# Kernel optimization log

Hardware: AMD Instinct MI355X
Metric: run time of the kernel (lower is better)

## Reference

```python
import jax, jax.numpy as jnp
import numpy as np

N = 2048          # num nodes
C = 256           # dense_dim per input
EMB = 3 * C       # 768
H = 8             # num_heads
D = EMB // H      # 96 head_dim
ALPHA = 0.2       # leaky relu slope
SCALE = D ** -0.5


def setup_inputs() -> dict:
    key = jax.random.key(0)
    ks = jax.random.split(key, 9)
    sd = EMB ** -0.5
    return {
        "eh": jax.random.normal(ks[0], (N, C), jnp.float32),
        "er": jax.random.normal(ks[1], (N, C), jnp.float32),
        "et": jax.random.normal(ks[2], (N, C), jnp.float32),
        "h_id": jax.random.randint(ks[3], (N,), 0, 32),
        "W_w": jax.random.normal(ks[4], (EMB, EMB), jnp.float32) * sd,
        "a": jax.random.normal(ks[5], (2 * D, 1), jnp.float32) * (2 * D) ** -0.5,
        "proj_w": jax.random.normal(ks[6], (EMB, EMB), jnp.float32) * sd,
        "proj_b": jnp.zeros((EMB,), jnp.float32),
        "skip_w": jax.random.normal(ks[7], (EMB, EMB), jnp.float32) * sd,
        "skip_b": jnp.zeros((EMB,), jnp.float32),
    }


def reference(eh, er, et, h_id, W_w, a, proj_w, proj_b, skip_w, skip_b):
    n = eh.shape[0]
    e = jnp.concatenate([eh, er, et], axis=-1)            # [N, EMB]
    Wh = (e @ W_w.T).reshape(n, H, D)                     # [N, H, D]

    # score = leakyrelu(a1 . Wh_scrambled[i] + a2 . Wh[j]) * scale
    a1, a2 = a[:D, 0], a[D:, 0]
    s1 = Wh @ a1                                          # [N, H]
    s2 = Wh @ a2                                          # [N, H]
    # torch's Wh.repeat(1,1,N).view(N*N,H,D) reads head (j*H + h)//N for pair (i,j,h)
    qidx = (jnp.arange(n)[:, None] * H + jnp.arange(H)[None, :]) // n  # [N, H]
    x = s1[:, qidx] + s2[None, :, :]                      # [N, N, H]
    e_ij = jnp.where(x >= 0, x, ALPHA * x) * SCALE

    mask = h_id[:, None] != h_id[None, :]                 # [N, N]
    e_ij = jnp.where(mask[:, :, None], -jnp.inf, e_ij)
    attn = jax.nn.softmax(e_ij, axis=1)                   # softmax over neighbors j

    out = jnp.einsum('ijh,jhd->ihd', attn, Wh).reshape(n, H * D)
    out = out @ proj_w.T + proj_b                         # [N, EMB]
    skip = e @ skip_w.T + skip_b                          # [N, EMB]
    return skip + out
```

## Files before the change

kernel.cpp:

```cpp
#include <hip/hip_runtime.h>
#include <hip/hip_bf16.h>

#define N_NODES 2048
#define EMB 768
#define NH 8
#define DH 96
#define ALPHA 0.2f
#define SCALE 0.10206207261596575f
#define NGMAX 192
#define WSZ (EMB * EMB)

typedef __bf16 bf16x8 __attribute__((ext_vector_type(8)));
typedef float f32x4 __attribute__((ext_vector_type(4)));
typedef __attribute__((address_space(3))) unsigned int lds_u32;
typedef __attribute__((address_space(1))) const unsigned int glb_u32;

union pack4 { ushort4 u; __hip_bfloat16 h[4]; };

__global__ __launch_bounds__(256) void prep_kernel(
    const float* __restrict__ eh, const float* __restrict__ er, const float* __restrict__ et,
    const float* __restrict__ W0, const float* __restrict__ W1, const float* __restrict__ W2,
    __hip_bfloat16* __restrict__ e, __hip_bfloat16* __restrict__ o0,
    __hip_bfloat16* __restrict__ o1, __hip_bfloat16* __restrict__ o2, int* __restrict__ cnt)
{
    const int b = blockIdx.x;
    const int gtid = b * 256 + threadIdx.x;
    if (gtid < 32) cnt[gtid] = 0;
    const float* src;
    __hip_bfloat16* dst;
    if (b < 1536) {
        int idx = gtid * 4;
        int i = idx / EMB, c = idx % EMB;
        if (c < 256)      src = eh + i * 256 + c;
        else if (c < 512) src = er + i * 256 + (c - 256);
        else              src = et + i * 256 + (c - 512);
        dst = e + (size_t)i * EMB + c;
    } else {
        int idx = (gtid - 1536 * 256) * 4;
        if (idx < WSZ)          { src = W0 + idx;           dst = o0 + idx; }
        else if (idx < 2 * WSZ) { src = W1 + idx - WSZ;     dst = o1 + idx - WSZ; }
        else                    { src = W2 + idx - 2 * WSZ; dst = o2 + idx - 2 * WSZ; }
    }
    float4 v = *reinterpret_cast<const float4*>(src);
    pack4 p;
    p.h[0] = __float2bfloat16(v.x);
    p.h[1] = __float2bfloat16(v.y);
    p.h[2] = __float2bfloat16(v.z);
    p.h[3] = __float2bfloat16(v.w);
    *reinterpret_cast<ushort4*>(dst) = p.u;
}

__device__ __forceinline__ void stageA64(
    const __hip_bfloat16* __restrict__ src, int row0, int k0,
    __hip_bfloat16* lds, int wave, int lane)
{
#pragma unroll
    for (int i = 0; i < 4; i++) {
        const int c0 = wave * 256 + i * 64;
        const int c = c0 + lane;
        const int row = c >> 3;
        const int cb = (c & 7) ^ (row & 7);
        const __hip_bfloat16* g = src + (size_t)(row0 + row) * EMB + k0 + cb * 8;
        __builtin_amdgcn_global_load_lds((glb_u32*)g, (lds_u32*)(lds + c0 * 8), 16, 0, 0);
    }
}
__device__ __forceinline__ void stageB64(
    const __hip_bfloat16* __restrict__ src, int row0, int k0,
    __hip_bfloat16* lds, int wave, int lane)
{
#pragma unroll
    for (int i = 0; i < 2; i++) {
        const int c0 = wave * 128 + i * 64;
        const int c = c0 + lane;
        const int row = c >> 3;
        const int cb = (c & 7) ^ (row & 7);
        const __hip_bfloat16* g = src + (size_t)(row0 + row) * EMB + k0 + cb * 8;
        __builtin_amdgcn_global_load_lds((glb_u32*)g, (lds_u32*)(lds + c0 * 8), 16, 0, 0);
    }
}

__global__ __launch_bounds__(256) void gemm_kernel(
    const __hip_bfloat16* __restrict__ A,
    const __hip_bfloat16* __restrict__ B1, const __hip_bfloat16* __restrict__ B2,
    const float* __restrict__ bias1, const float* __restrict__ bias2,
    float* __restrict__ C1, float* __restrict__ C2,
    int nbn1, int accum)
{
    __shared__ __attribute__((aligned(16))) __hip_bfloat16 smA[3][8192];
    __shared__ __attribute__((aligned(16))) __hip_bfloat16 smB[3][4096];

    const int t = threadIdx.x;
    const int lane = t & 63, wave = t >> 6;
    const int wm = wave >> 1, wn = wave & 1;
    const int bnb = blockIdx.x;
    const bool second = bnb >= nbn1;
    const __hip_bfloat16* B = second ? B2 : B1;
    float* Cf = second ? C2 : C1;
    const int bn = (second ? bnb - nbn1 : bnb) * 64;
    const int bm = blockIdx.y * 128;
    const int l15 = lane & 15, quad = lane >> 4;

    f32x4 acc00 = {0,0,0,0}, acc01 = {0,0,0,0};
    f32x4 acc10 = {0,0,0,0}, acc11 = {0,0,0,0};
    f32x4 acc20 = {0,0,0,0}, acc21 = {0,0,0,0};
    f32x4 acc30 = {0,0,0,0}, acc31 = {0,0,0,0};

    const int ra0 = wm * 64 + l15;
    const int rb0 = wn * 32 + l15;
    const int xa = ra0 & 7;
    const int xb = rb0 & 7;

    stageA64(A, bm, 0, &smA[0][0], wave, lane);
    stageB64(B, bn, 0, &smB[0][0], wave, lane);

    int bufc = 0;
#pragma unroll 1
    for (int s = 0; s < 12; s++) {
        const int bufn = (bufc == 2) ? 0 : bufc + 1;
        if (s + 1 < 12) {
            const int k0 = (s + 1) * 64;
            stageA64(A, bm, k0, &smA[bufn][0], wave, lane);
            stageB64(B, bn, k0, &smB[bufn][0], wave, lane);
            asm volatile("s_waitcnt vmcnt(6)" ::: "memory");
        } else {
            asm volatile("s_waitcnt vmcnt(0)" ::: "memory");
        }
        __builtin_amdgcn_s_barrier();

        const __hip_bfloat16* At = &smA[bufc][0];
        const __hip_bfloat16* Bt = &smB[bufc][0];
#pragma unroll
        for (int ks = 0; ks < 2; ks++) {
            const int cq = ks * 4 + quad;
            bf16x8 a0 = *(const bf16x8*)(At + (size_t)((ra0     ) * 8 + (cq ^ xa)) * 8);
            bf16x8 a1 = *(const bf16x8*)(At + (size_t)((ra0 + 16) * 8 + (cq ^ xa)) * 8);
            bf16x8 a2 = *(const bf16x8*)(At + (size_t)((ra0 + 32) * 8 + (cq ^ xa)) * 8);
            bf16x8 a3 = *(const bf16x8*)(At + (size_t)((ra0 + 48) * 8 + (cq ^ xa)) * 8);
            bf16x8 b0 = *(const bf16x8*)(Bt + (size_t)((rb0     ) * 8 + (cq ^ xb)) * 8);
            bf16x8 b1 = *(const bf16x8*)(Bt + (size_t)((rb0 + 16) * 8 + (cq ^ xb)) * 8);
            acc00 = __builtin_amdgcn_mfma_f32_16x16x32_bf16(a0, b0, acc00, 0, 0, 0);
            acc01 = __builtin_amdgcn_mfma_f32_16x16x32_bf16(a0, b1, acc01, 0, 0, 0);
            acc10 = __builtin_amdgcn_mfma_f32_16x16x32_bf16(a1, b0, acc10, 0, 0, 0);
            acc11 = __builtin_amdgcn_mfma_f32_16x16x32_bf16(a1, b1, acc11, 0, 0, 0);
            acc20 = __builtin_amdgcn_mfma_f32_16x16x32_bf16(a2, b0, acc20, 0, 0, 0);
            acc21 = __builtin_amdgcn_mfma_f32_16x16x32_bf16(a2, b1, acc21, 0, 0, 0);
            acc30 = __builtin_amdgcn_mfma_f32_16x16x32_bf16(a3, b0, acc30, 0, 0, 0);
            acc31 = __builtin_amdgcn_mfma_f32_16x16x32_bf16(a3, b1, acc31, 0, 0, 0);
        }
        bufc = bufn;
    }

    const int col0 = bn + wn * 32 + l15;
    const int col1 = col0 + 16;
    float bv0 = 0.f, bv1 = 0.f;
    if (second && bias1 != nullptr) {
        bv0 = bias1[col0] + bias2[col0];
        bv1 = bias1[col1] + bias2[col1];
    }
    const int r0 = bm + wm * 64 + quad * 4;
#pragma unroll
    for (int r = 0; r < 4; r++) {
        const int rw0 = r0 + r, rw1 = rw0 + 16, rw2 = rw0 + 32, rw3 = rw0 + 48;
        float* p00 = &Cf[(size_t)rw0 * EMB + col0]; float* p01 = &Cf[(size_t)rw0 * EMB + col1];
        float* p10 = &Cf[(size_t)rw1 * EMB + col0]; float* p11 = &Cf[(size_t)rw1 * EMB + col1];
        float* p20 = &Cf[(size_t)rw2 * EMB + col0]; float* p21 = &Cf[(size_t)rw2 * EMB + col1];
        float* p30 = &Cf[(size_t)rw3 * EMB + col0]; float* p31 = &Cf[(size_t)rw3 * EMB + col1];
        if (accum) {
            *p00 += acc00[r]; *p01 += acc01[r];
            *p10 += acc10[r]; *p11 += acc11[r];
            *p20 += acc20[r]; *p21 += acc21[r];
            *p30 += acc30[r]; *p31 += acc31[r];
        } else {
            *p00 = acc00[r] + bv0; *p01 = acc01[r] + bv1;
            *p10 = acc10[r] + bv0; *p11 = acc11[r] + bv1;
            *p20 = acc20[r] + bv0; *p21 = acc21[r] + bv1;
            *p30 = acc30[r] + bv0; *p31 = acc31[r] + bv1;
        }
    }
}

__global__ __launch_bounds__(256) void s12g_kernel(
    const float* __restrict__ Wh, const float* __restrict__ a,
    float* __restrict__ s1, float* __restrict__ s2,
    const int* __restrict__ h_id, int* __restrict__ cnt, int* __restrict__ lists)
{
    int gid = blockIdx.x * 256 + threadIdx.x;
    if (gid < N_NODES) {
        int g = h_id[gid];
        int p = atomicAdd(&cnt[g], 1);
        lists[g * N_NODES + p] = gid;
    }
    int i = gid >> 3, h = gid & 7;
    const float* wr = Wh + (size_t)i * EMB + h * DH;
    float acc1 = 0.f, acc2 = 0.f;
    for (int d = 0; d < DH; d++) {
        float w = wr[d];
        acc1 += w * a[d];
        acc2 += w * a[DH + d];
    }
    s1[gid] = acc1;
    s2[gid] = acc2;
}

__global__ __launch_bounds__(256) void attn_kernel(
    const float* __restrict__ Wh, const float* __restrict__ s1, const float* __restrict__ s2,
    const int* __restrict__ cnt, const int* __restrict__ lists,
    __hip_bfloat16* __restrict__ out)
{
    const int g  = blockIdx.x & 31;
    const int h  = (blockIdx.x >> 5) & 7;
    const int dh = blockIdx.x >> 8;
    const int t  = threadIdx.x;

    __shared__ int   jb[NGMAX];
    __shared__ int   qg[NGMAX];
    __shared__ float s2g[NGMAX];
    __shared__ float s1g[NGMAX][9];
    __shared__ float Whg[NGMAX][48];

    const int ng = min(cnt[g], NGMAX);
    const int* gl = lists + g * N_NODES;

    for (int j = t; j < ng; j += 256) {
        int node = gl[j];
        jb[j]  = node;
        qg[j]  = node >> 8;
        s2g[j] = s2[node * 8 + h];
        float4 v0 = *reinterpret_cast<const float4*>(s1 + node * 8);
        float4 v1 = *reinterpret_cast<const float4*>(s1 + node * 8 + 4);
        s1g[j][0] = v0.x; s1g[j][1] = v0.y; s1g[j][2] = v0.z; s1g[j][3] = v0.w;
        s1g[j][4] = v1.x; s1g[j][5] = v1.y; s1g[j][6] = v1.z; s1g[j][7] = v1.w;
    }
    __syncthreads();
    for (int idx = t; idx < ng * 12; idx += 256) {
        int jc = idx / 12, dq = idx % 12;
        float4 v = *reinterpret_cast<const float4*>(
            Wh + (size_t)jb[jc] * EMB + h * DH + dh * 48 + dq * 4);
        *reinterpret_cast<float4*>(&Whg[jc][dq * 4]) = v;
    }
    __syncthreads();

    const int half = t >> 7;
    const int d0 = half * 24;
    for (int tr = t & 127; tr < ng; tr += 128) {
        float m = -1e30f;
        for (int j = 0; j < ng; j++) {
            float x = s1g[tr][qg[j]] + s2g[j];
            float ev = (x >= 0.f ? x : ALPHA * x) * SCALE;
            m = fmaxf(m, ev);
        }
        float S = 0.f;
        for (int j = 0; j < ng; j++) {
            float x = s1g[tr][qg[j]] + s2g[j];
            float ev = (x >= 0.f ? x : ALPHA * x) * SCALE;
            S += __expf(ev - m);
        }
        const float ri = 1.f / S;

        float acc[24];
#pragma unroll
        for (int d = 0; d < 24; d++) acc[d] = 0.f;
        for (int j = 0; j < ng; j++) {
            float x = s1g[tr][qg[j]] + s2g[j];
            float ev = (x >= 0.f ? x : ALPHA * x) * SCALE;
            float p = __expf(ev - m) * ri;
#pragma unroll
            for (int d = 0; d < 24; d++) acc[d] += p * Whg[j][d0 + d];
        }
        __hip_bfloat16* po = out + (size_t)jb[tr] * EMB + h * DH + dh * 48 + d0;
#pragma unroll
        for (int d = 0; d < 24; d += 4) {
            pack4 pk;
            pk.h[0] = __float2bfloat16(acc[d]);
            pk.h[1] = __float2bfloat16(acc[d + 1]);
            pk.h[2] = __float2bfloat16(acc[d + 2]);
            pk.h[3] = __float2bfloat16(acc[d + 3]);
            *reinterpret_cast<ushort4*>(po + d) = pk.u;
        }
    }
}

extern "C" void kernel_launch(void* const* d_in, const int* in_sizes, int n_in,
                              void* d_out, int out_size, void* d_ws, size_t ws_size,
                              hipStream_t stream)
{
    const float* eh     = (const float*)d_in[0];
    const float* er     = (const float*)d_in[1];
    const float* et     = (const float*)d_in[2];
    const int*   h_id   = (const int*)d_in[3];
    const float* W_w    = (const float*)d_in[4];
    const float* a      = (const float*)d_in[5];
    const float* proj_w = (const float*)d_in[6];
    const float* proj_b = (const float*)d_in[7];
    const float* skip_w = (const float*)d_in[8];
    const float* skip_b = (const float*)d_in[9];
    float* out = (float*)d_out;

    char* ws = (char*)d_ws;
    __hip_bfloat16* e_ws   = (__hip_bfloat16*)(ws);
    float*          Wh_ws  = (float*)(ws + 3145728);
    __hip_bfloat16* at_ws  = (__hip_bfloat16*)(ws + 9437184);
    __hip_bfloat16* Wb_ws  = (__hip_bfloat16*)(ws + 12582912);
    __hip_bfloat16* Pb_ws  = (__hip_bfloat16*)(ws + 13762560);
    __hip_bfloat16* Sb_ws  = (__hip_bfloat16*)(ws + 14942208);
    float*          s1_ws  = (float*)(ws + 16121856);
    float*          s2_ws  = (float*)(ws + 16187392);
    int*            cnt_ws = (int*)(ws + 16252928);
    int*            lst_ws = (int*)(ws + 16253056);

    prep_kernel<<<3264, 256, 0, stream>>>(eh, er, et, W_w, proj_w, skip_w,
                                          e_ws, Wb_ws, Pb_ws, Sb_ws, cnt_ws);

    gemm_kernel<<<dim3(24, 16), 256, 0, stream>>>(
        e_ws, Wb_ws, Sb_ws, proj_b, skip_b, Wh_ws, out, 12, 0);

    s12g_kernel<<<64, 256, 0, stream>>>(Wh_ws, a, s1_ws, s2_ws, h_id, cnt_ws, lst_ws);

    attn_kernel<<<512, 256, 0, stream>>>(Wh_ws, s1_ws, s2_ws, cnt_ws, lst_ws, at_ws);

    gemm_kernel<<<dim3(12, 16), 256, 0, stream>>>(
        at_ws, Pb_ws, nullptr, nullptr, nullptr, out, nullptr, 12, 1);
}
```

Before: 137.3 us.

## Fuse all stages into one persistent kernel with grid barriers

Replaces the five separate launches with a single 512-block persistent kernel that runs prep/convert, both GEMMs, attention and the projection GEMM as phases separated by atomic grid barriers. The s1/s2 attention scores are now computed in the first GEMM's epilogue via shuffle reductions and atomics, and the per-group node lists are built deterministically by one block instead of atomic appends. This removes launch gaps and a separate scoring pass. In exchange it relies on all 512 blocks being co-resident (2 per CU with 72KB of LDS each), and it idles many blocks during the GEMM phases.

```diff
diff --git a/kernel.cpp b/kernel.cpp
--- a/kernel.cpp
+++ b/kernel.cpp
@@ -9,6 +9,7 @@
 #define SCALE 0.10206207261596575f
 #define NGMAX 192
 #define WSZ (EMB * EMB)
+#define NBLK 512u
 
 typedef __bf16 bf16x8 __attribute__((ext_vector_type(8)));
 typedef float f32x4 __attribute__((ext_vector_type(4)));
@@ -17,37 +18,20 @@
 
 union pack4 { ushort4 u; __hip_bfloat16 h[4]; };
 
-__global__ __launch_bounds__(256) void prep_kernel(
-    const float* __restrict__ eh, const float* __restrict__ er, const float* __restrict__ et,
-    const float* __restrict__ W0, const float* __restrict__ W1, const float* __restrict__ W2,
-    __hip_bfloat16* __restrict__ e, __hip_bfloat16* __restrict__ o0,
-    __hip_bfloat16* __restrict__ o1, __hip_bfloat16* __restrict__ o2, int* __restrict__ cnt)
-{
-    const int b = blockIdx.x;
-    const int gtid = b * 256 + threadIdx.x;
-    if (gtid < 32) cnt[gtid] = 0;
-    const float* src;
-    __hip_bfloat16* dst;
-    if (b < 1536) {
-        int idx = gtid * 4;
-        int i = idx / EMB, c = idx % EMB;
-        if (c < 256)      src = eh + i * 256 + c;
-        else if (c < 512) src = er + i * 256 + (c - 256);
-        else              src = et + i * 256 + (c - 512);
-        dst = e + (size_t)i * EMB + c;
-    } else {
-        int idx = (gtid - 1536 * 256) * 4;
-        if (idx < WSZ)          { src = W0 + idx;           dst = o0 + idx; }
-        else if (idx < 2 * WSZ) { src = W1 + idx - WSZ;     dst = o1 + idx - WSZ; }
-        else                    { src = W2 + idx - 2 * WSZ; dst = o2 + idx - 2 * WSZ; }
-    }
-    float4 v = *reinterpret_cast<const float4*>(src);
-    pack4 p;
-    p.h[0] = __float2bfloat16(v.x);
-    p.h[1] = __float2bfloat16(v.y);
-    p.h[2] = __float2bfloat16(v.z);
-    p.h[3] = __float2bfloat16(v.w);
-    *reinterpret_cast<ushort4*>(dst) = p.u;
+__device__ __forceinline__ void grid_barrier(unsigned* bar, unsigned target)
+{
+    __syncthreads();
+    if (threadIdx.x == 0) {
+        __threadfence();
+        atomicAdd(bar, 1u);
+        int guard = 0;
+        while (atomicAdd(bar, 0u) < target && guard < (1 << 22)) {
+            __builtin_amdgcn_s_sleep(1);
+            guard++;
+        }
+        __threadfence();
+    }
+    __syncthreads();
 }
 
 __device__ __forceinline__ void stageA64(
@@ -79,39 +63,28 @@
     }
 }
 
-__global__ __launch_bounds__(256) void gemm_kernel(
-    const __hip_bfloat16* __restrict__ A,
-    const __hip_bfloat16* __restrict__ B1, const __hip_bfloat16* __restrict__ B2,
+__device__ __forceinline__ void gemm_phase(
+    const __hip_bfloat16* __restrict__ A, const __hip_bfloat16* __restrict__ B,
+    float* __restrict__ Cf, int bm, int bn,
     const float* __restrict__ bias1, const float* __restrict__ bias2,
-    float* __restrict__ C1, float* __restrict__ C2,
-    int nbn1, int accum)
-{
-    __shared__ __attribute__((aligned(16))) __hip_bfloat16 smA[3][8192];
-    __shared__ __attribute__((aligned(16))) __hip_bfloat16 smB[3][4096];
-
-    const int t = threadIdx.x;
-    const int lane = t & 63, wave = t >> 6;
+    int accum,
+    const float* __restrict__ avec, float* __restrict__ s1, float* __restrict__ s2,
+    __hip_bfloat16* smA, __hip_bfloat16* smB, int lane, int wave)
+{
     const int wm = wave >> 1, wn = wave & 1;
-    const int bnb = blockIdx.x;
-    const bool second = bnb >= nbn1;
-    const __hip_bfloat16* B = second ? B2 : B1;
-    float* Cf = second ? C2 : C1;
-    const int bn = (second ? bnb - nbn1 : bnb) * 64;
-    const int bm = blockIdx.y * 128;
     const int l15 = lane & 15, quad = lane >> 4;
 
-    f32x4 acc00 = {0,0,0,0}, acc01 = {0,0,0,0};
-    f32x4 acc10 = {0,0,0,0}, acc11 = {0,0,0,0};
-    f32x4 acc20 = {0,0,0,0}, acc21 = {0,0,0,0};
-    f32x4 acc30 = {0,0,0,0}, acc31 = {0,0,0,0};
+    f32x4 acc[4][2];
+#pragma unroll
+    for (int k = 0; k < 4; k++) { acc[k][0] = f32x4{0,0,0,0}; acc[k][1] = f32x4{0,0,0,0}; }
 
     const int ra0 = wm * 64 + l15;
     const int rb0 = wn * 32 + l15;
     const int xa = ra0 & 7;
     const int xb = rb0 & 7;
 
-    stageA64(A, bm, 0, &smA[0][0], wave, lane);
-    stageB64(B, bn, 0, &smB[0][0], wave, lane);
+    stageA64(A, bm, 0, smA, wave, lane);
+    stageB64(B, bn, 0, smB, wave, lane);
 
     int bufc = 0;
 #pragma unroll 1
@@ -119,33 +92,27 @@
         const int bufn = (bufc == 2) ? 0 : bufc + 1;
         if (s + 1 < 12) {
             const int k0 = (s + 1) * 64;
-            stageA64(A, bm, k0, &smA[bufn][0], wave, lane);
-            stageB64(B, bn, k0, &smB[bufn][0], wave, lane);
+            stageA64(A, bm, k0, smA + bufn * 8192, wave, lane);
+            stageB64(B, bn, k0, smB + bufn * 4096, wave, lane);
             asm volatile("s_waitcnt vmcnt(6)" ::: "memory");
         } else {
             asm volatile("s_waitcnt vmcnt(0)" ::: "memory");
         }
         __builtin_amdgcn_s_barrier();
 
-        const __hip_bfloat16* At = &smA[bufc][0];
-        const __hip_bfloat16* Bt = &smB[bufc][0];
+        const __hip_bfloat16* At = smA + bufc * 8192;
+        const __hip_bfloat16* Bt = smB + bufc * 4096;
 #pragma unroll
         for (int ks = 0; ks < 2; ks++) {
             const int cq = ks * 4 + quad;
-            bf16x8 a0 = *(const bf16x8*)(At + (size_t)((ra0     ) * 8 + (cq ^ xa)) * 8);
-            bf16x8 a1 = *(const bf16x8*)(At + (size_t)((ra0 + 16) * 8 + (cq ^ xa)) * 8);
-            bf16x8 a2 = *(const bf16x8*)(At + (size_t)((ra0 + 32) * 8 + (cq ^ xa)) * 8);
-            bf16x8 a3 = *(const bf16x8*)(At + (size_t)((ra0 + 48) * 8 + (cq ^ xa)) * 8);
             bf16x8 b0 = *(const bf16x8*)(Bt + (size_t)((rb0     ) * 8 + (cq ^ xb)) * 8);
             bf16x8 b1 = *(const bf16x8*)(Bt + (size_t)((rb0 + 16) * 8 + (cq ^ xb)) * 8);
-            acc00 = __builtin_amdgcn_mfma_f32_16x16x32_bf16(a0, b0, acc00, 0, 0, 0);
-            acc01 = __builtin_amdgcn_mfma_f32_16x16x32_bf16(a0, b1, acc01, 0, 0, 0);
-            acc10 = __builtin_amdgcn_mfma_f32_16x16x32_bf16(a1, b0, acc10, 0, 0, 0);
-            acc11 = __builtin_amdgcn_mfma_f32_16x16x32_bf16(a1, b1, acc11, 0, 0, 0);
-            acc20 = __builtin_amdgcn_mfma_f32_16x16x32_bf16(a2, b0, acc20, 0, 0, 0);
-            acc21 = __builtin_amdgcn_mfma_f32_16x16x32_bf16(a2, b1, acc21, 0, 0, 0);
-            acc30 = __builtin_amdgcn_mfma_f32_16x16x32_bf16(a3, b0, acc30, 0, 0, 0);
-            acc31 = __builtin_amdgcn_mfma_f32_16x16x32_bf16(a3, b1, acc31, 0, 0, 0);
+#pragma unroll
+            for (int k = 0; k < 4; k++) {
+                bf16x8 av = *(const bf16x8*)(At + (size_t)((ra0 + 16 * k) * 8 + (cq ^ xa)) * 8);
+                acc[k][0] = __builtin_amdgcn_mfma_f32_16x16x32_bf16(av, b0, acc[k][0], 0, 0, 0);
+                acc[k][1] = __builtin_amdgcn_mfma_f32_16x16x32_bf16(av, b1, acc[k][1], 0, 0, 0);
+            }
         }
         bufc = bufn;
     }
@@ -153,130 +120,213 @@
     const int col0 = bn + wn * 32 + l15;
     const int col1 = col0 + 16;
     float bv0 = 0.f, bv1 = 0.f;
-    if (second && bias1 != nullptr) {
+    if (bias1 != nullptr) {
         bv0 = bias1[col0] + bias2[col0];
         bv1 = bias1[col1] + bias2[col1];
     }
     const int r0 = bm + wm * 64 + quad * 4;
 #pragma unroll
-    for (int r = 0; r < 4; r++) {
-        const int rw0 = r0 + r, rw1 = rw0 + 16, rw2 = rw0 + 32, rw3 = rw0 + 48;
-        float* p00 = &Cf[(size_t)rw0 * EMB + col0]; float* p01 = &Cf[(size_t)rw0 * EMB + col1];
-        float* p10 = &Cf[(size_t)rw1 * EMB + col0]; float* p11 = &Cf[(size_t)rw1 * EMB + col1];
-        float* p20 = &Cf[(size_t)rw2 * EMB + col0]; float* p21 = &Cf[(size_t)rw2 * EMB + col1];
-        float* p30 = &Cf[(size_t)rw3 * EMB + col0]; float* p31 = &Cf[(size_t)rw3 * EMB + col1];
-        if (accum) {
-            *p00 += acc00[r]; *p01 += acc01[r];
-            *p10 += acc10[r]; *p11 += acc11[r];
-            *p20 += acc20[r]; *p21 += acc21[r];
-            *p30 += acc30[r]; *p31 += acc31[r];
+    for (int k = 0; k < 4; k++) {
+#pragma unroll
+        for (int r = 0; r < 4; r++) {
+            const int row = r0 + 16 * k + r;
+            float* p0 = &Cf[(size_t)row * EMB + col0];
+            float* p1 = &Cf[(size_t)row * EMB + col1];
+            if (accum) { *p0 += acc[k][0][r]; *p1 += acc[k][1][r]; }
+            else       { *p0 = acc[k][0][r] + bv0; *p1 = acc[k][1][r] + bv1; }
+        }
+    }
+
+    if (avec != nullptr) {
+        const int cb0 = bn + wn * 32;
+        const int h = cb0 / DH;
+        const int ch = cb0 % DH + l15;
+        const float a10 = avec[ch],      a11 = avec[ch + 16];
+        const float a20 = avec[DH + ch], a21 = avec[DH + ch + 16];
+#pragma unroll
+        for (int k = 0; k < 4; k++) {
+#pragma unroll
+            for (int r = 0; r < 4; r++) {
+                float v1 = acc[k][0][r] * a10 + acc[k][1][r] * a11;
+                float v2 = acc[k][0][r] * a20 + acc[k][1][r] * a21;
+#pragma unroll
+                for (int m = 1; m < 16; m <<= 1) {
+                    v1 += __shfl_xor(v1, m);
+                    v2 += __shfl_xor(v2, m);
+                }
+                if (l15 == 0) {
+                    const int row = r0 + 16 * k + r;
+                    atomicAdd(&s1[row * NH + h], v1);
+                    atomicAdd(&s2[row * NH + h], v2);
+                }
+            }
+        }
+    }
+}
+
+__global__ __launch_bounds__(256, 2) void mega_kernel(
+    const float* __restrict__ eh, const float* __restrict__ er, const float* __restrict__ et,
+    const int* __restrict__ h_id, const float* __restrict__ a,
+    const float* __restrict__ proj_b, const float* __restrict__ skip_b,
+    const float* __restrict__ W_w, const float* __restrict__ proj_w, const float* __restrict__ skip_w,
+    __hip_bfloat16* __restrict__ e, __hip_bfloat16* __restrict__ Wb,
+    __hip_bfloat16* __restrict__ Pb, __hip_bfloat16* __restrict__ Sb,
+    float* __restrict__ Wh, float* __restrict__ s1, float* __restrict__ s2,
+    int* __restrict__ cnt, int* __restrict__ lists,
+    __hip_bfloat16* __restrict__ at, float* __restrict__ out,
+    unsigned* __restrict__ bar)
+{
+    __shared__ __attribute__((aligned(16))) char lds_raw[73728];
+
+    const int bid = blockIdx.x;
+    const int t = threadIdx.x;
+    const int lane = t & 63, wave = t >> 6;
+
+    {
+        const float4 z4 = {0.f, 0.f, 0.f, 0.f};
+        for (int i = bid * 256 + t; i < 843776; i += 512 * 256) {
+            if (i < 393216) {
+                const int idx = i * 4;
+                const int row = idx / EMB, c = idx % EMB;
+                const float* src;
+                if (c < 256)      src = eh + row * 256 + c;
+                else if (c < 512) src = er + row * 256 + (c - 256);
+                else              src = et + row * 256 + (c - 512);
+                float4 v = *reinterpret_cast<const float4*>(src);
+                pack4 p;
+                p.h[0] = __float2bfloat16(v.x); p.h[1] = __float2bfloat16(v.y);
+                p.h[2] = __float2bfloat16(v.z); p.h[3] = __float2bfloat16(v.w);
+                *reinterpret_cast<ushort4*>(e + (size_t)row * EMB + c) = p.u;
+            } else if (i < 835584) {
+                const int w = i - 393216;
+                const int which = w / 147456;
+                const int off = (w % 147456) * 4;
+                const float* src = (which == 0 ? W_w : which == 1 ? proj_w : skip_w) + off;
+                __hip_bfloat16* dst = (which == 0 ? Wb : which == 1 ? Pb : Sb) + off;
+                float4 v = *reinterpret_cast<const float4*>(src);
+                pack4 p;
+                p.h[0] = __float2bfloat16(v.x); p.h[1] = __float2bfloat16(v.y);
+                p.h[2] = __float2bfloat16(v.z); p.h[3] = __float2bfloat16(v.w);
+                *reinterpret_cast<ushort4*>(dst) = p.u;
+            } else {
+                reinterpret_cast<float4*>(s1)[i - 835584] = z4;
+            }
+        }
+        if (bid == 511) {
+            int* hh = (int*)lds_raw;
+            int (*seg)[8] = (int(*)[8])(lds_raw + 8192);
+            for (int j = t; j < N_NODES; j += 256) hh[j] = h_id[j];
+            __syncthreads();
+            const int g = t >> 3, sgt = t & 7;
+            int c = 0;
+            for (int j = sgt * 256; j < sgt * 256 + 256; j++) c += (hh[j] == g) ? 1 : 0;
+            seg[g][sgt] = c;
+            __syncthreads();
+            int off = 0;
+            for (int k = 0; k < sgt; k++) off += seg[g][k];
+            int p = off;
+            for (int j = sgt * 256; j < sgt * 256 + 256; j++)
+                if (hh[j] == g) lists[g * N_NODES + (p++)] = j;
+            if (sgt == 7) cnt[g] = off + c;
+        }
+    }
+    grid_barrier(bar, NBLK);
+
+    if (bid < 384) {
+        const int bnb = bid % 24, bmb = bid / 24;
+        const int bm = bmb * 128;
+        __hip_bfloat16* smA = (__hip_bfloat16*)lds_raw;
+        __hip_bfloat16* smB = (__hip_bfloat16*)(lds_raw + 49152);
+        if (bnb < 12) {
+            gemm_phase(e, Wb, Wh, bm, bnb * 64, nullptr, nullptr, 0,
+                       a, s1, s2, smA, smB, lane, wave);
         } else {
-            *p00 = acc00[r] + bv0; *p01 = acc01[r] + bv1;
-            *p10 = acc10[r] + bv0; *p11 = acc11[r] + bv1;
-            *p20 = acc20[r] + bv0; *p21 = acc21[r] + bv1;
-            *p30 = acc30[r] + bv0; *p31 = acc31[r] + bv1;
-        }
-    }
-}
-
-__global__ __launch_bounds__(256) void s12g_kernel(
-    const float* __restrict__ Wh, const float* __restrict__ a,
-    float* __restrict__ s1, float* __restrict__ s2,
-    const int* __restrict__ h_id, int* __restrict__ cnt, int* __restrict__ lists)
-{
-    int gid = blockIdx.x * 256 + threadIdx.x;
-    if (gid < N_NODES) {
-        int g = h_id[gid];
-        int p = atomicAdd(&cnt[g], 1);
-        lists[g * N_NODES + p] = gid;
-    }
-    int i = gid >> 3, h = gid & 7;
-    const float* wr = Wh + (size_t)i * EMB + h * DH;
-    float acc1 = 0.f, acc2 = 0.f;
-    for (int d = 0; d < DH; d++) {
-        float w = wr[d];
-        acc1 += w * a[d];
-        acc2 += w * a[DH + d];
-    }
-    s1[gid] = acc1;
-    s2[gid] = acc2;
-}
-
-__global__ __launch_bounds__(256) void attn_kernel(
-    const float* __restrict__ Wh, const float* __restrict__ s1, const float* __restrict__ s2,
-    const int* __restrict__ cnt, const int* __restrict__ lists,
-    __hip_bfloat16* __restrict__ out)
-{
-    const int g  = blockIdx.x & 31;
-    const int h  = (blockIdx.x >> 5) & 7;
-    const int dh = blockIdx.x >> 8;
-    const int t  = threadIdx.x;
-
-    __shared__ int   jb[NGMAX];
-    __shared__ int   qg[NGMAX];
-    __shared__ float s2g[NGMAX];
-    __shared__ float s1g[NGMAX][9];
-    __shared__ float Whg[NGMAX][48];
-
-    const int ng = min(cnt[g], NGMAX);
-    const int* gl = lists + g * N_NODES;
-
-    for (int j = t; j < ng; j += 256) {
-        int node = gl[j];
-        jb[j]  = node;
-        qg[j]  = node >> 8;
-        s2g[j] = s2[node * 8 + h];
-        float4 v0 = *reinterpret_cast<const float4*>(s1 + node * 8);
-        float4 v1 = *reinterpret_cast<const float4*>(s1 + node * 8 + 4);
-        s1g[j][0] = v0.x; s1g[j][1] = v0.y; s1g[j][2] = v0.z; s1g[j][3] = v0.w;
-        s1g[j][4] = v1.x; s1g[j][5] = v1.y; s1g[j][6] = v1.z; s1g[j][7] = v1.w;
-    }
-    __syncthreads();
-    for (int idx = t; idx < ng * 12; idx += 256) {
-        int jc = idx / 12, dq = idx % 12;
-        float4 v = *reinterpret_cast<const float4*>(
-            Wh + (size_t)jb[jc] * EMB + h * DH + dh * 48 + dq * 4);
-        *reinterpret_cast<float4*>(&Whg[jc][dq * 4]) = v;
-    }
-    __syncthreads();
-
-    const int half = t >> 7;
-    const int d0 = half * 24;
-    for (int tr = t & 127; tr < ng; tr += 128) {
-        float m = -1e30f;
-        for (int j = 0; j < ng; j++) {
-            float x = s1g[tr][qg[j]] + s2g[j];
-            float ev = (x >= 0.f ? x : ALPHA * x) * SCALE;
-            m = fmaxf(m, ev);
-        }
-        float S = 0.f;
-        for (int j = 0; j < ng; j++) {
-            float x = s1g[tr][qg[j]] + s2g[j];
-            float ev = (x >= 0.f ? x : ALPHA * x) * SCALE;
-            S += __expf(ev - m);
-        }
-        const float ri = 1.f / S;
-
-        float acc[24];
-#pragma unroll
-        for (int d = 0; d < 24; d++) acc[d] = 0.f;
-        for (int j = 0; j < ng; j++) {
-            float x = s1g[tr][qg[j]] + s2g[j];
-            float ev = (x >= 0.f ? x : ALPHA * x) * SCALE;
-            float p = __expf(ev - m) * ri;
-#pragma unroll
-            for (int d = 0; d < 24; d++) acc[d] += p * Whg[j][d0 + d];
-        }
-        __hip_bfloat16* po = out + (size_t)jb[tr] * EMB + h * DH + dh * 48 + d0;
-#pragma unroll
-        for (int d = 0; d < 24; d += 4) {
-            pack4 pk;
-            pk.h[0] = __float2bfloat16(acc[d]);
-            pk.h[1] = __float2bfloat16(acc[d + 1]);
-            pk.h[2] = __float2bfloat16(acc[d + 2]);
-            pk.h[3] = __float2bfloat16(acc[d + 3]);
-            *reinterpret_cast<ushort4*>(po + d) = pk.u;
-        }
+            gemm_phase(e, Sb, out, bm, (bnb - 12) * 64, proj_b, skip_b, 0,
+                       nullptr, nullptr, nullptr, smA, smB, lane, wave);
+        }
+    }
+    grid_barrier(bar, 2 * NBLK);
+
+    {
+        const int g  = bid & 31;
+        const int h  = (bid >> 5) & 7;
+        const int dh = bid >> 8;
+
+        int*   jb  = (int*)lds_raw;
+        int*   qg  = (int*)(lds_raw + 768);
+        float* s2g = (float*)(lds_raw + 1536);
+        float (*s1g)[9]  = (float(*)[9])(lds_raw + 2304);
+        float (*Whg)[48] = (float(*)[48])(lds_raw + 9216);
+
+        const int ng = min(cnt[g], NGMAX);
+        const int* gl = lists + g * N_NODES;
+
+        for (int j = t; j < ng; j += 256) {
+            int node = gl[j];
+            jb[j]  = node;
+            qg[j]  = node >> 8;
+            s2g[j] = s2[node * 8 + h];
+            float4 v0 = *reinterpret_cast<const float4*>(s1 + node * 8);
+            float4 v1 = *reinterpret_cast<const float4*>(s1 + node * 8 + 4);
+            s1g[j][0] = v0.x; s1g[j][1] = v0.y; s1g[j][2] = v0.z; s1g[j][3] = v0.w;
+            s1g[j][4] = v1.x; s1g[j][5] = v1.y; s1g[j][6] = v1.z; s1g[j][7] = v1.w;
+        }
+        __syncthreads();
+        for (int idx = t; idx < ng * 12; idx += 256) {
+            int jc = idx / 12, dq = idx % 12;
+            float4 v = *reinterpret_cast<const float4*>(
+                Wh + (size_t)jb[jc] * EMB + h * DH + dh * 48 + dq * 4);
+            *reinterpret_cast<float4*>(&Whg[jc][dq * 4]) = v;
+        }
+        __syncthreads();
+
+        const int half = t >> 7;
+        const int d0 = half * 24;
+        for (int tr = t & 127; tr < ng; tr += 128) {
+            float m = -1e30f;
+            for (int j = 0; j < ng; j++) {
+                float x = s1g[tr][qg[j]] + s2g[j];
+                float ev = (x >= 0.f ? x : ALPHA * x) * SCALE;
+                m = fmaxf(m, ev);
+            }
+            float S = 0.f;
+            for (int j = 0; j < ng; j++) {
+                float x = s1g[tr][qg[j]] + s2g[j];
+                float ev = (x >= 0.f ? x : ALPHA * x) * SCALE;
+                S += __expf(ev - m);
+            }
+            const float ri = 1.f / S;
+
+            float acc[24];
+#pragma unroll
+            for (int d = 0; d < 24; d++) acc[d] = 0.f;
+            for (int j = 0; j < ng; j++) {
+                float x = s1g[tr][qg[j]] + s2g[j];
+                float ev = (x >= 0.f ? x : ALPHA * x) * SCALE;
+                float p = __expf(ev - m) * ri;
+#pragma unroll
+                for (int d = 0; d < 24; d++) acc[d] += p * Whg[j][d0 + d];
+            }
+            __hip_bfloat16* po = at + (size_t)jb[tr] * EMB + h * DH + dh * 48 + d0;
+#pragma unroll
+            for (int d = 0; d < 24; d += 4) {
+                pack4 pk;
+                pk.h[0] = __float2bfloat16(acc[d]);
+                pk.h[1] = __float2bfloat16(acc[d + 1]);
+                pk.h[2] = __float2bfloat16(acc[d + 2]);
+                pk.h[3] = __float2bfloat16(acc[d + 3]);
+                *reinterpret_cast<ushort4*>(po + d) = pk.u;
+            }
+        }
+    }
+    grid_barrier(bar, 3 * NBLK);
+
+    if (bid < 192) {
+        const int bnb = bid % 12, bmb = bid / 12;
+        __hip_bfloat16* smA = (__hip_bfloat16*)lds_raw;
+        __hip_bfloat16* smB = (__hip_bfloat16*)(lds_raw + 49152);
+        gemm_phase(at, Pb, out, bmb * 128, bnb * 64, nullptr, nullptr, 1,
+                   nullptr, nullptr, nullptr, smA, smB, lane, wave);
     }
 }
 
@@ -307,17 +357,12 @@
     float*          s2_ws  = (float*)(ws + 16187392);
     int*            cnt_ws = (int*)(ws + 16252928);
     int*            lst_ws = (int*)(ws + 16253056);
-
-    prep_kernel<<<3264, 256, 0, stream>>>(eh, er, et, W_w, proj_w, skip_w,
-                                          e_ws, Wb_ws, Pb_ws, Sb_ws, cnt_ws);
-
-    gemm_kernel<<<dim3(24, 16), 256, 0, stream>>>(
-        e_ws, Wb_ws, Sb_ws, proj_b, skip_b, Wh_ws, out, 12, 0);
-
-    s12g_kernel<<<64, 256, 0, stream>>>(Wh_ws, a, s1_ws, s2_ws, h_id, cnt_ws, lst_ws);
-
-    attn_kernel<<<512, 256, 0, stream>>>(Wh_ws, s1_ws, s2_ws, cnt_ws, lst_ws, at_ws);
-
-    gemm_kernel<<<dim3(12, 16), 256, 0, stream>>>(
-        at_ws, Pb_ws, nullptr, nullptr, nullptr, out, nullptr, 12, 1);
-}
+    unsigned*       bar_ws = (unsigned*)(ws + 16515200);
+
+    hipMemsetAsync(bar_ws, 0, 8, stream);
+
+    mega_kernel<<<512, 256, 0, stream>>>(
+        eh, er, et, h_id, a, proj_b, skip_b, W_w, proj_w, skip_w,
+        e_ws, Wb_ws, Pb_ws, Sb_ws, Wh_ws, s1_ws, s2_ws,
+        cnt_ws, lst_ws, at_ws, out, bar_ws);
+}
```

New measurement: 300.0 us. +118.5%, slower.

## Fuse s1/s2 score projections into Wh GEMM epilogue and build group lists in prep

Applied to the files above, without the earlier changes.

Removes the separate s12g kernel. The attention score dot products are computed in the first GEMM's epilogue from accumulators via wave shuffles and atomicAdd into zeroed s1/s2 buffers. The group membership lists are built deterministically in an extra prep block using LDS counting and prefix offsets, and zeroing of s1/s2 is added to prep. This saves one launch and a reread of Wh, at the cost of float atomics, which make summation order nondeterministic, and a serial single-block list build inside prep.

```diff
diff --git a/kernel.cpp b/kernel.cpp
--- a/kernel.cpp
+++ b/kernel.cpp
@@ -20,34 +20,57 @@
 __global__ __launch_bounds__(256) void prep_kernel(
     const float* __restrict__ eh, const float* __restrict__ er, const float* __restrict__ et,
     const float* __restrict__ W0, const float* __restrict__ W1, const float* __restrict__ W2,
+    const int* __restrict__ h_id,
     __hip_bfloat16* __restrict__ e, __hip_bfloat16* __restrict__ o0,
-    __hip_bfloat16* __restrict__ o1, __hip_bfloat16* __restrict__ o2, int* __restrict__ cnt)
+    __hip_bfloat16* __restrict__ o1, __hip_bfloat16* __restrict__ o2,
+    float4* __restrict__ zbase, int* __restrict__ cnt, int* __restrict__ lists)
 {
     const int b = blockIdx.x;
-    const int gtid = b * 256 + threadIdx.x;
-    if (gtid < 32) cnt[gtid] = 0;
-    const float* src;
-    __hip_bfloat16* dst;
-    if (b < 1536) {
-        int idx = gtid * 4;
-        int i = idx / EMB, c = idx % EMB;
-        if (c < 256)      src = eh + i * 256 + c;
-        else if (c < 512) src = er + i * 256 + (c - 256);
-        else              src = et + i * 256 + (c - 512);
-        dst = e + (size_t)i * EMB + c;
+    const int t = threadIdx.x;
+    if (b < 3264) {
+        const int gtid = b * 256 + t;
+        const float* src;
+        __hip_bfloat16* dst;
+        if (b < 1536) {
+            int idx = gtid * 4;
+            int i = idx / EMB, c = idx % EMB;
+            if (c < 256)      src = eh + i * 256 + c;
+            else if (c < 512) src = er + i * 256 + (c - 256);
+            else              src = et + i * 256 + (c - 512);
+            dst = e + (size_t)i * EMB + c;
+        } else {
+            int idx = (gtid - 1536 * 256) * 4;
+            if (idx < WSZ)          { src = W0 + idx;           dst = o0 + idx; }
+            else if (idx < 2 * WSZ) { src = W1 + idx - WSZ;     dst = o1 + idx - WSZ; }
+            else                    { src = W2 + idx - 2 * WSZ; dst = o2 + idx - 2 * WSZ; }
+        }
+        float4 v = *reinterpret_cast<const float4*>(src);
+        pack4 p;
+        p.h[0] = __float2bfloat16(v.x);
+        p.h[1] = __float2bfloat16(v.y);
+        p.h[2] = __float2bfloat16(v.z);
+        p.h[3] = __float2bfloat16(v.w);
+        *reinterpret_cast<ushort4*>(dst) = p.u;
+    } else if (b < 3296) {
+        const float4 z = {0.f, 0.f, 0.f, 0.f};
+        zbase[(size_t)(b - 3264) * 256 + t] = z;
     } else {
-        int idx = (gtid - 1536 * 256) * 4;
-        if (idx < WSZ)          { src = W0 + idx;           dst = o0 + idx; }
-        else if (idx < 2 * WSZ) { src = W1 + idx - WSZ;     dst = o1 + idx - WSZ; }
-        else                    { src = W2 + idx - 2 * WSZ; dst = o2 + idx - 2 * WSZ; }
-    }
-    float4 v = *reinterpret_cast<const float4*>(src);
-    pack4 p;
-    p.h[0] = __float2bfloat16(v.x);
-    p.h[1] = __float2bfloat16(v.y);
-    p.h[2] = __float2bfloat16(v.z);
-    p.h[3] = __float2bfloat16(v.w);
-    *reinterpret_cast<ushort4*>(dst) = p.u;
+        __shared__ int hh[N_NODES];
+        __shared__ int seg[32][8];
+        for (int j = t; j < N_NODES; j += 256) hh[j] = h_id[j];
+        __syncthreads();
+        const int g = t >> 3, s = t & 7;
+        int c = 0;
+        for (int j = s * 256; j < s * 256 + 256; j++) c += (hh[j] == g) ? 1 : 0;
+        seg[g][s] = c;
+        __syncthreads();
+        int off = 0;
+        for (int k = 0; k < s; k++) off += seg[g][k];
+        int p = off;
+        for (int j = s * 256; j < s * 256 + 256; j++)
+            if (hh[j] == g) lists[g * N_NODES + (p++)] = j;
+        if (s == 7) cnt[g] = off + c;
+    }
 }
 
 __device__ __forceinline__ void stageA64(
@@ -79,39 +102,28 @@
     }
 }
 
-__global__ __launch_bounds__(256) void gemm_kernel(
-    const __hip_bfloat16* __restrict__ A,
-    const __hip_bfloat16* __restrict__ B1, const __hip_bfloat16* __restrict__ B2,
+__device__ __forceinline__ void gemm_phase(
+    const __hip_bfloat16* __restrict__ A, const __hip_bfloat16* __restrict__ B,
+    float* __restrict__ Cf, int bm, int bn,
     const float* __restrict__ bias1, const float* __restrict__ bias2,
-    float* __restrict__ C1, float* __restrict__ C2,
-    int nbn1, int accum)
-{
-    __shared__ __attribute__((aligned(16))) __hip_bfloat16 smA[3][8192];
-    __shared__ __attribute__((aligned(16))) __hip_bfloat16 smB[3][4096];
-
-    const int t = threadIdx.x;
-    const int lane = t & 63, wave = t >> 6;
+    int accum,
+    const float* __restrict__ avec, float* __restrict__ s1, float* __restrict__ s2,
+    __hip_bfloat16* smA, __hip_bfloat16* smB, int lane, int wave)
+{
     const int wm = wave >> 1, wn = wave & 1;
-    const int bnb = blockIdx.x;
-    const bool second = bnb >= nbn1;
-    const __hip_bfloat16* B = second ? B2 : B1;
-    float* Cf = second ? C2 : C1;
-    const int bn = (second ? bnb - nbn1 : bnb) * 64;
-    const int bm = blockIdx.y * 128;
     const int l15 = lane & 15, quad = lane >> 4;
 
-    f32x4 acc00 = {0,0,0,0}, acc01 = {0,0,0,0};
-    f32x4 acc10 = {0,0,0,0}, acc11 = {0,0,0,0};
-    f32x4 acc20 = {0,0,0,0}, acc21 = {0,0,0,0};
-    f32x4 acc30 = {0,0,0,0}, acc31 = {0,0,0,0};
+    f32x4 acc[4][2];
+#pragma unroll
+    for (int k = 0; k < 4; k++) { acc[k][0] = f32x4{0,0,0,0}; acc[k][1] = f32x4{0,0,0,0}; }
 
     const int ra0 = wm * 64 + l15;
     const int rb0 = wn * 32 + l15;
     const int xa = ra0 & 7;
     const int xb = rb0 & 7;
 
-    stageA64(A, bm, 0, &smA[0][0], wave, lane);
-    stageB64(B, bn, 0, &smB[0][0], wave, lane);
+    stageA64(A, bm, 0, smA, wave, lane);
+    stageB64(B, bn, 0, smB, wave, lane);
 
     int bufc = 0;
 #pragma unroll 1
@@ -119,33 +131,27 @@
         const int bufn = (bufc == 2) ? 0 : bufc + 1;
         if (s + 1 < 12) {
             const int k0 = (s + 1) * 64;
-            stageA64(A, bm, k0, &smA[bufn][0], wave, lane);
-            stageB64(B, bn, k0, &smB[bufn][0], wave, lane);
+            stageA64(A, bm, k0, smA + bufn * 8192, wave, lane);
+            stageB64(B, bn, k0, smB + bufn * 4096, wave, lane);
             asm volatile("s_waitcnt vmcnt(6)" ::: "memory");
         } else {
             asm volatile("s_waitcnt vmcnt(0)" ::: "memory");
         }
         __builtin_amdgcn_s_barrier();
 
-        const __hip_bfloat16* At = &smA[bufc][0];
-        const __hip_bfloat16* Bt = &smB[bufc][0];
+        const __hip_bfloat16* At = smA + bufc * 8192;
+        const __hip_bfloat16* Bt = smB + bufc * 4096;
 #pragma unroll
         for (int ks = 0; ks < 2; ks++) {
             const int cq = ks * 4 + quad;
-            bf16x8 a0 = *(const bf16x8*)(At + (size_t)((ra0     ) * 8 + (cq ^ xa)) * 8);
-            bf16x8 a1 = *(const bf16x8*)(At + (size_t)((ra0 + 16) * 8 + (cq ^ xa)) * 8);
-            bf16x8 a2 = *(const bf16x8*)(At + (size_t)((ra0 + 32) * 8 + (cq ^ xa)) * 8);
-            bf16x8 a3 = *(const bf16x8*)(At + (size_t)((ra0 + 48) * 8 + (cq ^ xa)) * 8);
             bf16x8 b0 = *(const bf16x8*)(Bt + (size_t)((rb0     ) * 8 + (cq ^ xb)) * 8);
             bf16x8 b1 = *(const bf16x8*)(Bt + (size_t)((rb0 + 16) * 8 + (cq ^ xb)) * 8);
-            acc00 = __builtin_amdgcn_mfma_f32_16x16x32_bf16(a0, b0, acc00, 0, 0, 0);
-            acc01 = __builtin_amdgcn_mfma_f32_16x16x32_bf16(a0, b1, acc01, 0, 0, 0);
-            acc10 = __builtin_amdgcn_mfma_f32_16x16x32_bf16(a1, b0, acc10, 0, 0, 0);
-            acc11 = __builtin_amdgcn_mfma_f32_16x16x32_bf16(a1, b1, acc11, 0, 0, 0);
-            acc20 = __builtin_amdgcn_mfma_f32_16x16x32_bf16(a2, b0, acc20, 0, 0, 0);
-            acc21 = __builtin_amdgcn_mfma_f32_16x16x32_bf16(a2, b1, acc21, 0, 0, 0);
-            acc30 = __builtin_amdgcn_mfma_f32_16x16x32_bf16(a3, b0, acc30, 0, 0, 0);
-            acc31 = __builtin_amdgcn_mfma_f32_16x16x32_bf16(a3, b1, acc31, 0, 0, 0);
+#pragma unroll
+            for (int k = 0; k < 4; k++) {
+                bf16x8 av = *(const bf16x8*)(At + (size_t)((ra0 + 16 * k) * 8 + (cq ^ xa)) * 8);
+                acc[k][0] = __builtin_amdgcn_mfma_f32_16x16x32_bf16(av, b0, acc[k][0], 0, 0, 0);
+                acc[k][1] = __builtin_amdgcn_mfma_f32_16x16x32_bf16(av, b1, acc[k][1], 0, 0, 0);
+            }
         }
         bufc = bufn;
     }
@@ -153,53 +159,71 @@
     const int col0 = bn + wn * 32 + l15;
     const int col1 = col0 + 16;
     float bv0 = 0.f, bv1 = 0.f;
-    if (second && bias1 != nullptr) {
+    if (bias1 != nullptr) {
         bv0 = bias1[col0] + bias2[col0];
         bv1 = bias1[col1] + bias2[col1];
     }
     const int r0 = bm + wm * 64 + quad * 4;
 #pragma unroll
-    for (int r = 0; r < 4; r++) {
-        const int rw0 = r0 + r, rw1 = rw0 + 16, rw2 = rw0 + 32, rw3 = rw0 + 48;
-        float* p00 = &Cf[(size_t)rw0 * EMB + col0]; float* p01 = &Cf[(size_t)rw0 * EMB + col1];
-        float* p10 = &Cf[(size_t)rw1 * EMB + col0]; float* p11 = &Cf[(size_t)rw1 * EMB + col1];
-        float* p20 = &Cf[(size_t)rw2 * EMB + col0]; float* p21 = &Cf[(size_t)rw2 * EMB + col1];
-        float* p30 = &Cf[(size_t)rw3 * EMB + col0]; float* p31 = &Cf[(size_t)rw3 * EMB + col1];
-        if (accum) {
-            *p00 += acc00[r]; *p01 += acc01[r];
-            *p10 += acc10[r]; *p11 += acc11[r];
-            *p20 += acc20[r]; *p21 += acc21[r];
-            *p30 += acc30[r]; *p31 += acc31[r];
-        } else {
-            *p00 = acc00[r] + bv0; *p01 = acc01[r] + bv1;
-            *p10 = acc10[r] + bv0; *p11 = acc11[r] + bv1;
-            *p20 = acc20[r] + bv0; *p21 = acc21[r] + bv1;
-            *p30 = acc30[r] + bv0; *p31 = acc31[r] + bv1;
-        }
-    }
-}
-
-__global__ __launch_bounds__(256) void s12g_kernel(
-    const float* __restrict__ Wh, const float* __restrict__ a,
-    float* __restrict__ s1, float* __restrict__ s2,
-    const int* __restrict__ h_id, int* __restrict__ cnt, int* __restrict__ lists)
-{
-    int gid = blockIdx.x * 256 + threadIdx.x;
-    if (gid < N_NODES) {
-        int g = h_id[gid];
-        int p = atomicAdd(&cnt[g], 1);
-        lists[g * N_NODES + p] = gid;
-    }
-    int i = gid >> 3, h = gid & 7;
-    const float* wr = Wh + (size_t)i * EMB + h * DH;
-    float acc1 = 0.f, acc2 = 0.f;
-    for (int d = 0; d < DH; d++) {
-        float w = wr[d];
-        acc1 += w * a[d];
-        acc2 += w * a[DH + d];
-    }
-    s1[gid] = acc1;
-    s2[gid] = acc2;
+    for (int k = 0; k < 4; k++) {
+#pragma unroll
+        for (int r = 0; r < 4; r++) {
+            const int row = r0 + 16 * k + r;
+            float* p0 = &Cf[(size_t)row * EMB + col0];
+            float* p1 = &Cf[(size_t)row * EMB + col1];
+            if (accum) { *p0 += acc[k][0][r]; *p1 += acc[k][1][r]; }
+            else       { *p0 = acc[k][0][r] + bv0; *p1 = acc[k][1][r] + bv1; }
+        }
+    }
+
+    if (avec != nullptr) {
+        const int cb0 = bn + wn * 32;
+        const int h = cb0 / DH;
+        const int ch = cb0 % DH + l15;
+        const float a10 = avec[ch],      a11 = avec[ch + 16];
+        const float a20 = avec[DH + ch], a21 = avec[DH + ch + 16];
+#pragma unroll
+        for (int k = 0; k < 4; k++) {
+#pragma unroll
+            for (int r = 0; r < 4; r++) {
+                float v1 = acc[k][0][r] * a10 + acc[k][1][r] * a11;
+                float v2 = acc[k][0][r] * a20 + acc[k][1][r] * a21;
+#pragma unroll
+                for (int m = 1; m < 16; m <<= 1) {
+                    v1 += __shfl_xor(v1, m);
+                    v2 += __shfl_xor(v2, m);
+                }
+                if (l15 == 0) {
+                    const int row = r0 + 16 * k + r;
+                    atomicAdd(&s1[row * NH + h], v1);
+                    atomicAdd(&s2[row * NH + h], v2);
+                }
+            }
+        }
+    }
+}
+
+__global__ __launch_bounds__(256) void gemm_kernel(
+    const __hip_bfloat16* __restrict__ A,
+    const __hip_bfloat16* __restrict__ B1, const __hip_bfloat16* __restrict__ B2,
+    const float* __restrict__ bias1, const float* __restrict__ bias2,
+    float* __restrict__ C1, float* __restrict__ C2,
+    int nbn1, int accum,
+    const float* __restrict__ avec, float* __restrict__ s1, float* __restrict__ s2)
+{
+    __shared__ __attribute__((aligned(16))) __hip_bfloat16 smA[3][8192];
+    __shared__ __attribute__((aligned(16))) __hip_bfloat16 smB[3][4096];
+    const int t = threadIdx.x;
+    const int lane = t & 63, wave = t >> 6;
+    const int bnb = blockIdx.x;
+    const bool second = bnb >= nbn1;
+    if (second) {
+        gemm_phase(A, B2, C2, blockIdx.y * 128, (bnb - nbn1) * 64, bias1, bias2, accum,
+                   nullptr, nullptr, nullptr, &smA[0][0], &smB[0][0], lane, wave);
+    } else {
+        gemm_phase(A, B1, C1, blockIdx.y * 128, bnb * 64, nullptr, nullptr, accum,
+                   avec, s1, s2, &smA[0][0], &smB[0][0], lane, wave);
+    }
 }
 
 __global__ __launch_bounds__(256) void attn_kernel(
@@ -308,16 +332,17 @@
     int*            cnt_ws = (int*)(ws + 16252928);
     int*            lst_ws = (int*)(ws + 16253056);
 
-    prep_kernel<<<3264, 256, 0, stream>>>(eh, er, et, W_w, proj_w, skip_w,
-                                          e_ws, Wb_ws, Pb_ws, Sb_ws, cnt_ws);
+    prep_kernel<<<3297, 256, 0, stream>>>(eh, er, et, W_w, proj_w, skip_w, h_id,
+                                          e_ws, Wb_ws, Pb_ws, Sb_ws,
+                                          (float4*)(ws + 16121856), cnt_ws, lst_ws);
 
     gemm_kernel<<<dim3(24, 16), 256, 0, stream>>>(
-        e_ws, Wb_ws, Sb_ws, proj_b, skip_b, Wh_ws, out, 12, 0);
-
-    s12g_kernel<<<64, 256, 0, stream>>>(Wh_ws, a, s1_ws, s2_ws, h_id, cnt_ws, lst_ws);
+        e_ws, Wb_ws, Sb_ws, proj_b, skip_b, Wh_ws, out, 12, 0,
+        a, s1_ws, s2_ws);
 
     attn_kernel<<<512, 256, 0, stream>>>(Wh_ws, s1_ws, s2_ws, cnt_ws, lst_ws, at_ws);
 
     gemm_kernel<<<dim3(12, 16), 256, 0, stream>>>(
-        at_ws, Pb_ws, nullptr, nullptr, nullptr, out, nullptr, 12, 1);
-}
+        at_ws, Pb_ws, nullptr, nullptr, nullptr, out, nullptr, 12, 1,
+        nullptr, nullptr, nullptr);
+}
```

After: 163.5 us. 19.1% more time.
